# Kernel optimization log

Measured on AMD Instinct MI355X. Metric: run time of the kernel, lower is better.

## Reference

```python
import jax, jax.numpy as jnp
import numpy as np
from jax.scipy.stats import norm

N = 6144
D1, D2 = 3000, 1000
H = 128          # hardcoded hidden in VAEEncoder
LAT = 64
E = 16           # num_experts
K = 2            # top-k
NOISE_EPS = 0.01
BN_EPS = 1e-5


def setup_inputs() -> dict:
    key = jax.random.key(0)
    ks = jax.random.split(key, 24)
    xav = lambda k, i, o: jax.random.uniform(k, (i, o), jnp.float32,
                                             -np.sqrt(6.0 / (i + o)), np.sqrt(6.0 / (i + o)))
    u = jax.random.uniform(ks[0], (N, N), jnp.float32)
    adj = u / u.sum(axis=1, keepdims=True)  # row-normalized dense graph
    inp = {
        'x1': jax.random.normal(ks[1], (N, D1), jnp.float32),
        'x2': jax.random.normal(ks[2], (N, D2), jnp.float32),
        'adj': adj,
        # modality-1 VAE encoder
        'W1': xav(ks[3], D1, H), 'gamma1': jnp.ones((H,)), 'beta1': jnp.zeros((H,)),
        'Wmu1': xav(ks[4], H, LAT), 'bmu1': jnp.zeros((LAT,)),
        'Wlv1': xav(ks[5], H, LAT), 'blv1': jnp.zeros((LAT,)),
        # modality-2 VAE encoder
        'W2': xav(ks[6], D2, H), 'gamma2': jnp.ones((H,)), 'beta2': jnp.zeros((H,)),
        'Wmu2': xav(ks[7], H, LAT), 'bmu2': jnp.zeros((LAT,)),
        'Wlv2': xav(ks[8], H, LAT), 'blv2': jnp.zeros((LAT,)),
        # MoE gating (torch inits these to zero; small randn gives a non-degenerate baseline)
        'w_gate': 0.02 * jax.random.normal(ks[9], (LAT, E), jnp.float32),
        'w_noise': 0.02 * jax.random.normal(ks[10], (LAT, E), jnp.float32),
        # modality decoders
        'Wd1': xav(ks[11], LAT, LAT), 'Wfc1': xav(ks[12], LAT, D1), 'bfc1': jnp.zeros((D1,)),
        'Wd2': xav(ks[13], LAT, LAT), 'Wfc2': xav(ks[14], LAT, D2), 'bfc2': jnp.zeros((D2,)),
    }
    return inp


def _encode(x, adj, W, gamma, beta, Wmu, bmu, Wlv, blv):
    h = adj @ (x @ W)                                   # [N,H] GNN embed
    mu_b = h.mean(0)
    var_b = h.var(0)
    h = (h - mu_b) / jnp.sqrt(var_b + BN_EPS) * gamma + beta  # BatchNorm1d (train mode)
    return h @ Wmu + bmu, h @ Wlv + blv                 # mu, logvar [N,LAT]


def _cv_squared(v):
    return v.var(ddof=1) / (v.mean() ** 2 + 1e-10)


def _moe_gating(z, w_gate, w_noise, key):
    clean = z @ w_gate                                  # [N,E]
    std = jax.nn.softplus(z @ w_noise) + NOISE_EPS
    noisy = clean + jax.random.normal(key, clean.shape, clean.dtype) * std
    top_vals, top_idx = jax.lax.top_k(noisy, K + 1)     # [N,K+1]
    topk_gates = jax.nn.softmax(top_vals[:, :K], axis=1)
    rows = jnp.arange(z.shape[0])[:, None]
    gates = jnp.zeros_like(clean).at[rows, top_idx[:, :K]].set(topk_gates)
    # differentiable load estimate (prob each expert is in top-k)
    thr_in = top_vals[:, K][:, None]
    thr_out = top_vals[:, K - 1][:, None]
    is_in = noisy > thr_in
    prob = jnp.where(is_in, norm.cdf((clean - thr_in) / std), norm.cdf((clean - thr_out) / std))
    load = prob.sum(0)
    importance = gates.sum(0)
    loss = _cv_squared(importance) + _cv_squared(load)
    return gates, loss


def _decode(z, adj, Wd, Wfc, bfc):
    return (adj @ (z @ Wd)) @ Wfc + bfc                 # Decoder: mm, mm, Linear


def reference(x1, x2, adj,
              W1, gamma1, beta1, Wmu1, bmu1, Wlv1, blv1,
              W2, gamma2, beta2, Wmu2, bmu2, Wlv2, blv2,
              w_gate, w_noise,
              Wd1, Wfc1, bfc1, Wd2, Wfc2, bfc2):
    mu1, lv1 = _encode(x1, adj, W1, gamma1, beta1, Wmu1, bmu1, Wlv1, blv1)
    mu2, lv2 = _encode(x2, adj, W2, gamma2, beta2, Wmu2, bmu2, Wlv2, blv2)
    # Product of Experts over the 2 modalities
    mus = jnp.stack([mu1, mu2], 0)
    lvs = jnp.stack([lv1, lv2], 0)
    var = jnp.exp(lvs) + 1e-8
    T = 1.0 / (var + 1e-8)
    pd_mu = (mus * T).sum(0) / T.sum(0)
    pd_logvar = jnp.log(1.0 / T.sum(0) + 1e-8)
    z = pd_mu
    gates, moe_loss = _moe_gating(z, w_gate, w_noise, jax.random.key(42))
    recon1 = _decode(z, adj, Wd1, Wfc1, bfc1)
    recon2 = _decode(z, adj, Wd2, Wfc2, bfc2)
    return recon1, recon2, pd_mu, pd_logvar, gates, moe_loss
```

## Files before the change

### kernel.cpp

```cpp
#include <hip/hip_runtime.h>
#include <math.h>

#define NR    6144
#define DIM1  3000
#define DIM2  1000
#define HID   128
#define LATD  64
#define NEXP  16

typedef __bf16 bf16x8 __attribute__((ext_vector_type(8)));
typedef float  f32x4  __attribute__((ext_vector_type(4)));

__device__ __forceinline__ unsigned short f2bf_rne(float x) {
  unsigned u = __float_as_uint(x);
  u += 0x7FFFu + ((u >> 16) & 1u);
  return (unsigned short)(u >> 16);
}
__device__ __forceinline__ void split2(float v, unsigned short& h, unsigned short& l) {
  h = f2bf_rne(v);
  float hf = __uint_as_float((unsigned)h << 16);
  l = f2bf_rne(v - hf);
}

template<bool SPLIT3, bool ATOMIC>
__device__ __forceinline__ void gemm_body(
    unsigned short* __restrict__ bufA, unsigned short* __restrict__ bufB,
    const float* __restrict__ A,
    const unsigned short* __restrict__ BTh,
    const unsigned short* __restrict__ BTl,
    const float* __restrict__ bias,
    float* __restrict__ C,
    int M, int N, int K, int lda, int Kpad, int ldc,
    int bm, int bn, int k0, int kend)
{
  const int tid  = threadIdx.x;
  const int lane = tid & 63;
  const int wave = tid >> 6;
  const int wm = wave >> 1, wn = wave & 1;
  const int lrow = lane & 15, kg = lane >> 4;
  const int nsteps = (kend - k0 + 31) >> 5;

  f32x4 acc[4][4];
  #pragma unroll
  for (int f = 0; f < 4; ++f)
    #pragma unroll
    for (int g = 0; g < 4; ++g)
      #pragma unroll
      for (int j = 0; j < 4; ++j) acc[f][g][j] = 0.f;

  const int srow = tid >> 1;
  const int ks   = (tid & 1) * 16;
  const int s0   = (tid & 1) * 2;
  const float* aRow = A + (size_t)(bm + srow) * lda;
  const int gn = bn + srow;
  const bool bvalid = gn < N;
  const unsigned short* bRowH = BTh + (size_t)(bvalid ? gn : 0) * Kpad;
  const unsigned short* bRowL = SPLIT3 ? (BTl + (size_t)(bvalid ? gn : 0) * Kpad) : BTh;

  const int rx = srow & 7;
  const int wa0 = srow * 64 + (((s0 + 0) ^ rx) * 8);
  const int wa1 = srow * 64 + (((s0 + 1) ^ rx) * 8);
  const int wa2 = srow * 64 + (((s0 + 4) ^ rx) * 8);
  const int wa3 = srow * 64 + (((s0 + 5) ^ rx) * 8);

  float va[16];
  uint4 bh0 = make_uint4(0,0,0,0), bh1 = bh0, bl0 = bh0, bl1 = bh0;

  auto loadA = [&](int gk) {
    const int kb = gk + ks;
    if (kb + 16 <= kend) {
      const float4* ap = (const float4*)(aRow + kb);
      #pragma unroll
      for (int q = 0; q < 4; ++q) {
        float4 f4 = ap[q];
        va[4*q+0] = f4.x; va[4*q+1] = f4.y; va[4*q+2] = f4.z; va[4*q+3] = f4.w;
      }
    } else {
      #pragma unroll
      for (int i = 0; i < 16; ++i) va[i] = (kb + i < kend) ? aRow[kb + i] : 0.f;
    }
  };
  auto loadB = [&](int gk) {
    if (bvalid) {
      const uint4* bp = (const uint4*)(bRowH + gk + ks);
      bh0 = bp[0]; bh1 = bp[1];
      if (SPLIT3) {
        const uint4* bq = (const uint4*)(bRowL + gk + ks);
        bl0 = bq[0]; bl1 = bq[1];
      }
    }
  };

  loadA(k0);
  loadB(k0);

  for (int s = 0; s < nsteps; ++s) {
    const int gk = k0 + s * 32;

    unsigned hw[8], lw[8];
    #pragma unroll
    for (int i = 0; i < 8; ++i) {
      if (SPLIT3) {
        unsigned short h0, l0, h1, l1;
        split2(va[2*i], h0, l0);
        split2(va[2*i+1], h1, l1);
        hw[i] = (unsigned)h0 | ((unsigned)h1 << 16);
        lw[i] = (unsigned)l0 | ((unsigned)l1 << 16);
      } else {
        hw[i] = (unsigned)f2bf_rne(va[2*i]) | ((unsigned)f2bf_rne(va[2*i+1]) << 16);
        lw[i] = 0;
      }
    }

    __syncthreads();
    *(uint4*)&bufA[wa0] = make_uint4(hw[0], hw[1], hw[2], hw[3]);
    *(uint4*)&bufA[wa1] = make_uint4(hw[4], hw[5], hw[6], hw[7]);
    if (SPLIT3) {
      *(uint4*)&bufA[wa2] = make_uint4(lw[0], lw[1], lw[2], lw[3]);
      *(uint4*)&bufA[wa3] = make_uint4(lw[4], lw[5], lw[6], lw[7]);
      *(uint4*)&bufB[wa0] = bh0;
      *(uint4*)&bufB[wa1] = bh1;
      *(uint4*)&bufB[wa2] = bl0;
      *(uint4*)&bufB[wa3] = bl1;
    } else {
      *(uint4*)&bufA[wa2] = bh0;
      *(uint4*)&bufA[wa3] = bh1;
    }
    __syncthreads();

    if (s + 1 < nsteps) {
      loadA(gk + 32);
      loadB(gk + 32);
    }

    bf16x8 afh[4], bfh[4], afl[4], bfl[4];
    #pragma unroll
    for (int f = 0; f < 4; ++f) {
      const int r = wm * 64 + f * 16 + lrow;
      afh[f] = *(const bf16x8*)&bufA[r * 64 + ((kg ^ (r & 7)) * 8)];
      if (SPLIT3) afl[f] = *(const bf16x8*)&bufA[r * 64 + (((4 + kg) ^ (r & 7)) * 8)];
      const int n = wn * 64 + f * 16 + lrow;
      if (SPLIT3) {
        bfh[f] = *(const bf16x8*)&bufB[n * 64 + ((kg ^ (n & 7)) * 8)];
        bfl[f] = *(const bf16x8*)&bufB[n * 64 + (((4 + kg) ^ (n & 7)) * 8)];
      } else {
        bfh[f] = *(const bf16x8*)&bufA[n * 64 + (((4 + kg) ^ (n & 7)) * 8)];
      }
    }
    #pragma unroll
    for (int f = 0; f < 4; ++f)
      #pragma unroll
      for (int g = 0; g < 4; ++g) {
        acc[f][g] = __builtin_amdgcn_mfma_f32_16x16x32_bf16(afh[f], bfh[g], acc[f][g], 0, 0, 0);
        if constexpr (SPLIT3) {
          acc[f][g] = __builtin_amdgcn_mfma_f32_16x16x32_bf16(afl[f], bfh[g], acc[f][g], 0, 0, 0);
          acc[f][g] = __builtin_amdgcn_mfma_f32_16x16x32_bf16(afh[f], bfl[g], acc[f][g], 0, 0, 0);
        }
      }
  }

  #pragma unroll
  for (int f = 0; f < 4; ++f) {
    #pragma unroll
    for (int g = 0; g < 4; ++g) {
      const int row0 = bm + wm * 64 + f * 16 + (lane >> 4) * 4;
      const int col  = bn + wn * 64 + g * 16 + (lane & 15);
      if (col < N) {
        #pragma unroll
        for (int j = 0; j < 4; ++j) {
          const size_t idx = (size_t)(row0 + j) * ldc + col;
          if (ATOMIC) atomicAdd(&C[idx], acc[f][g][j]);
          else        C[idx] = acc[f][g][j] + (bias ? bias[col] : 0.f);
        }
      }
    }
  }
}

template<bool SPLIT3, bool ATOMIC>
__global__ __launch_bounds__(256, 3) void gemm_mfma(
    const float* __restrict__ A,
    const unsigned short* __restrict__ BTh,
    const unsigned short* __restrict__ BTl,
    const float* __restrict__ bias,
    float* __restrict__ C,
    int M, int N, int K, int lda, int Kpad, int ldc, int kchunk)
{
  __shared__ alignas(16) unsigned short bufA[128 * 64];
  __shared__ alignas(16) unsigned short bufB[SPLIT3 ? 128 * 64 : 8];
  const int k0 = blockIdx.z * kchunk;
  gemm_body<SPLIT3, ATOMIC>(bufA, bufB, A, BTh, BTl, bias, C,
                            M, N, K, lda, Kpad, ldc,
                            blockIdx.x * 128, blockIdx.y * 128,
                            k0, min(k0 + kchunk, K));
}

__global__ __launch_bounds__(256, 3) void gemm_enc(
    const float* __restrict__ x1,
    const unsigned short* __restrict__ W1h, const unsigned short* __restrict__ W1l,
    const float* __restrict__ x2,
    const unsigned short* __restrict__ W2h, const unsigned short* __restrict__ W2l,
    float* __restrict__ XW)
{
  __shared__ alignas(16) unsigned short bufA[128 * 64];
  __shared__ alignas(16) unsigned short bufB[128 * 64];
  if (blockIdx.y == 0) {
    const int k0 = blockIdx.z * 376;
    gemm_body<true, true>(bufA, bufB, x1, W1h, W1l, nullptr, XW,
                          NR, HID, DIM1, DIM1, 3008, 256,
                          blockIdx.x * 128, 0, k0, min(k0 + 376, DIM1));
  } else {
    const int k0 = blockIdx.z * 128;
    gemm_body<true, true>(bufA, bufB, x2, W2h, W2l, nullptr, XW + HID,
                          NR, HID, DIM2, DIM2, 1024, 256,
                          blockIdx.x * 128, 0, k0, min(k0 + 128, DIM2));
  }
}

__global__ __launch_bounds__(256) void transpose_split(
    const float* __restrict__ in, unsigned short* __restrict__ out_hi,
    unsigned short* __restrict__ out_lo, int K, int N, int Kpad)
{
  __shared__ float tile[32][33];
  const int k0 = blockIdx.x * 32, n0 = blockIdx.y * 32;
  const int tx = threadIdx.x & 31, ty = threadIdx.x >> 5;
  #pragma unroll
  for (int r = 0; r < 4; ++r) {
    const int k = k0 + ty + r * 8;
    tile[ty + r * 8][tx] = (k < K && n0 + tx < N) ? in[(size_t)k * N + n0 + tx] : 0.f;
  }
  __syncthreads();
  #pragma unroll
  for (int r = 0; r < 4; ++r) {
    const int nn = ty + r * 8;
    const int n = n0 + nn, k = k0 + tx;
    if (n < N && k < Kpad) {
      unsigned short h, l;
      split2(tile[tx][nn], h, l);
      out_hi[(size_t)n * Kpad + k] = h;
      if (out_lo) out_lo[(size_t)n * Kpad + k] = l;
    }
  }
}

#define BM 64
#define BN 64
#define BK 16

__global__ __launch_bounds__(256) void gemm_f32(
    const float* __restrict__ A, const float* __restrict__ B,
    const float* __restrict__ bias, float* __restrict__ C,
    int M, int N, int K, int lda, int ldb, int ldc)
{
  __shared__ float At[BK][BM + 4];
  __shared__ float Bt[BK][BN + 4];
  const int tid = threadIdx.x;
  const int tx = tid & 15;
  const int ty = tid >> 4;
  const int bm = blockIdx.x * BM;
  const int bn = blockIdx.y * BN;

  float acc[4][4] = {};

  const int ar = tid >> 2;
  const int ak = (tid & 3) * 4;
  const int bk = tid >> 4;
  const int bc = (tid & 15) * 4;

  for (int k0 = 0; k0 < K; k0 += BK) {
    {
      float4 v = make_float4(0.f, 0.f, 0.f, 0.f);
      const int gr = bm + ar;
      const int gk = k0 + ak;
      if (gr < M && gk < K) {
        const float* p = &A[(size_t)gr * lda];
        if (gk + 3 < K) v = *reinterpret_cast<const float4*>(&p[gk]);
        else {
          v.x = p[gk];
          if (gk + 1 < K) v.y = p[gk + 1];
          if (gk + 2 < K) v.z = p[gk + 2];
        }
      }
      At[ak + 0][ar] = v.x; At[ak + 1][ar] = v.y;
      At[ak + 2][ar] = v.z; At[ak + 3][ar] = v.w;
    }
    {
      float4 v = make_float4(0.f, 0.f, 0.f, 0.f);
      const int gk = k0 + bk;
      const int gc = bn + bc;
      if (gk < K) {
        const float* p = &B[(size_t)gk * ldb];
        if (gc + 3 < N) v = *reinterpret_cast<const float4*>(&p[gc]);
        else {
          if (gc     < N) v.x = p[gc];
          if (gc + 1 < N) v.y = p[gc + 1];
          if (gc + 2 < N) v.z = p[gc + 2];
        }
      }
      *reinterpret_cast<float4*>(&Bt[bk][bc]) = v;
    }
    __syncthreads();
    #pragma unroll
    for (int kk = 0; kk < BK; ++kk) {
      float4 a4 = *reinterpret_cast<const float4*>(&At[kk][ty * 4]);
      float4 b4 = *reinterpret_cast<const float4*>(&Bt[kk][tx * 4]);
      float av[4] = {a4.x, a4.y, a4.z, a4.w};
      float bv[4] = {b4.x, b4.y, b4.z, b4.w};
      #pragma unroll
      for (int i = 0; i < 4; ++i)
        #pragma unroll
        for (int j = 0; j < 4; ++j)
          acc[i][j] = fmaf(av[i], bv[j], acc[i][j]);
    }
    __syncthreads();
  }

  #pragma unroll
  for (int i = 0; i < 4; ++i) {
    const int row = bm + ty * 4 + i;
    if (row >= M) continue;
    #pragma unroll
    for (int j = 0; j < 4; ++j) {
      const int col = bn + tx * 4 + j;
      if (col < N) {
        float v = acc[i][j];
        if (bias) v += bias[col];
        C[(size_t)row * ldc + col] = v;
      }
    }
  }
}

__global__ __launch_bounds__(256) void bnstats_kernel(
    const float* __restrict__ H2, float* __restrict__ ssum, float* __restrict__ ssq)
{
  const int c = threadIdx.x;
  const int r0 = blockIdx.x * 12;
  float s = 0.f, q = 0.f;
  #pragma unroll
  for (int i = 0; i < 12; ++i) {
    float v = H2[(size_t)(r0 + i) * 256 + c];
    s += v;
    q = fmaf(v, v, q);
  }
  atomicAdd(&ssum[c], s);
  atomicAdd(&ssq[c], q);
}

__global__ __launch_bounds__(256) void mulv_kernel(
    const float* __restrict__ H2, const float* __restrict__ ssum, const float* __restrict__ ssq,
    const float* __restrict__ g1, const float* __restrict__ b1,
    const float* __restrict__ Wmu1, const float* __restrict__ bmu1,
    const float* __restrict__ Wlv1, const float* __restrict__ blv1,
    const float* __restrict__ g2, const float* __restrict__ b2,
    const float* __restrict__ Wmu2, const float* __restrict__ bmu2,
    const float* __restrict__ Wlv2, const float* __restrict__ blv2,
    float* __restrict__ pd_mu_out, float* __restrict__ pd_lv_out, float* __restrict__ z_out)
{
  __shared__ float hn[4][256];
  const int tid = threadIdx.x;
  const int r0 = blockIdx.x * 4;

  for (int idx = tid; idx < 1024; idx += 256) {
    const int rr = idx >> 8;
    const int c  = idx & 255;
    const float mean = ssum[c] * (1.0f / 6144.0f);
    const float var  = ssq[c] * (1.0f / 6144.0f) - mean * mean;
    const float rstd = 1.0f / sqrtf(var + 1e-5f);
    const float gamma = (c < HID) ? g1[c] : g2[c - HID];
    const float beta  = (c < HID) ? b1[c] : b2[c - HID];
    const float v = H2[(size_t)(r0 + rr) * 256 + c];
    hn[rr][c] = (v - mean) * rstd * gamma + beta;
  }
  __syncthreads();

  const int rr = tid >> 6;
  const int j  = tid & 63;
  float mu1 = bmu1[j], lv1 = blv1[j], mu2 = bmu2[j], lv2 = blv2[j];
  #pragma unroll 4
  for (int k = 0; k < HID; ++k) {
    const float h1 = hn[rr][k];
    const float h2 = hn[rr][HID + k];
    mu1 = fmaf(h1, Wmu1[k * LATD + j], mu1);
    lv1 = fmaf(h1, Wlv1[k * LATD + j], lv1);
    mu2 = fmaf(h2, Wmu2[k * LATD + j], mu2);
    lv2 = fmaf(h2, Wlv2[k * LATD + j], lv2);
  }
  const float var1 = expf(lv1) + 1e-8f;
  const float var2 = expf(lv2) + 1e-8f;
  const float T1 = 1.0f / (var1 + 1e-8f);
  const float T2 = 1.0f / (var2 + 1e-8f);
  const float denom = T1 + T2;
  const float pmu = (mu1 * T1 + mu2 * T2) / denom;
  const float plv = logf(1.0f / denom + 1e-8f);
  const size_t o = (size_t)(r0 + rr) * LATD + j;
  pd_mu_out[o] = pmu;
  pd_lv_out[o] = plv;
  z_out[o]     = pmu;
}

__device__ __forceinline__ unsigned rotl32(unsigned x, int r) {
  return (x << r) | (x >> (32 - r));
}

__device__ float threefry_normal(unsigned i) {
  const unsigned ks0 = 0u;
  const unsigned ks1 = 42u;
  const unsigned ks2 = 0x1BD11BDAu ^ 0u ^ 42u;
  unsigned x0 = 0u + ks0;
  unsigned x1 = i + ks1;

  #define TF_ROUND(r) { x0 += x1; x1 = rotl32(x1, r); x1 ^= x0; }
  TF_ROUND(13) TF_ROUND(15) TF_ROUND(26) TF_ROUND(6)
  x0 += ks1; x1 += ks2 + 1u;
  TF_ROUND(17) TF_ROUND(29) TF_ROUND(16) TF_ROUND(24)
  x0 += ks2; x1 += ks0 + 2u;
  TF_ROUND(13) TF_ROUND(15) TF_ROUND(26) TF_ROUND(6)
  x0 += ks0; x1 += ks1 + 3u;
  TF_ROUND(17) TF_ROUND(29) TF_ROUND(16) TF_ROUND(24)
  x0 += ks1; x1 += ks2 + 4u;
  TF_ROUND(13) TF_ROUND(15) TF_ROUND(26) TF_ROUND(6)
  x0 += ks2; x1 += ks0 + 5u;
  #undef TF_ROUND

  const unsigned bits = x0 ^ x1;

  const unsigned fb = (bits >> 9) | 0x3F800000u;
  const float u01 = __uint_as_float(fb) - 1.0f;
  const float minval = -0.99999994f;
  float u = fmaf(u01, 2.0f, minval);
  u = fmaxf(minval, u);

  float w = -log1pf(-u * u);
  float p;
  if (w < 5.0f) {
    w = w - 2.5f;
    p = 2.81022636e-08f;
    p = fmaf(p, w, 3.43273939e-07f);
    p = fmaf(p, w, -3.5233877e-06f);
    p = fmaf(p, w, -4.39150654e-06f);
    p = fmaf(p, w, 0.00021858087f);
    p = fmaf(p, w, -0.00125372503f);
    p = fmaf(p, w, -0.00417768164f);
    p = fmaf(p, w, 0.246640727f);
    p = fmaf(p, w, 1.50140941f);
  } else {
    w = sqrtf(w) - 3.0f;
    p = -0.000200214257f;
    p = fmaf(p, w, 0.000100950558f);
    p = fmaf(p, w, 0.00134934322f);
    p = fmaf(p, w, -0.00367342844f);
    p = fmaf(p, w, 0.00573950773f);
    p = fmaf(p, w, -0.0076224613f);
    p = fmaf(p, w, 0.00943887047f);
    p = fmaf(p, w, 1.00167406f);
    p = fmaf(p, w, 2.83297682f);
  }
  return 1.4142135f * (p * u);
}

__global__ __launch_bounds__(64) void gating_kernel(
    const float* __restrict__ z, const float* __restrict__ w_gate,
    const float* __restrict__ w_noise, float* __restrict__ gates_out,
    float* __restrict__ importance, float* __restrict__ loadv)
{
  __shared__ float zt[64][65];
  __shared__ float wg[64][16];
  __shared__ float wn[64][16];
  __shared__ float imp_s[16];
  __shared__ float load_s[16];

  const int tid = threadIdx.x;
  const int r0 = blockIdx.x * 64;

  for (int idx = tid; idx < 1024; idx += 64) {
    wg[idx >> 4][idx & 15] = w_gate[idx];
    wn[idx >> 4][idx & 15] = w_noise[idx];
  }
  for (int idx = tid; idx < 4096; idx += 64) {
    const int rr = idx >> 6, c = idx & 63;
    zt[rr][c] = z[(size_t)(r0 + rr) * 64 + c];
  }
  if (tid < 16) { imp_s[tid] = 0.f; load_s[tid] = 0.f; }
  __syncthreads();

  const int r = r0 + tid;
  float clean[16], noisy[16], stdv[16];
  #pragma unroll
  for (int e = 0; e < NEXP; ++e) {
    float c = 0.f, n = 0.f;
    #pragma unroll 8
    for (int k = 0; k < 64; ++k) {
      const float zv = zt[tid][k];
      c = fmaf(zv, wg[k][e], c);
      n = fmaf(zv, wn[k][e], n);
    }
    clean[e] = c;
    const float sp = fmaxf(n, 0.f) + log1pf(expf(-fabsf(n)));
    stdv[e] = sp + 0.01f;
    const float eps = threefry_normal((unsigned)r * 16u + (unsigned)e);
    noisy[e] = fmaf(eps, stdv[e], c);
  }

  float v0 = -1e30f, v1 = -1e30f, v2 = -1e30f;
  int i0 = 0, i1 = 0;
  #pragma unroll
  for (int e = 0; e < NEXP; ++e) {
    const float v = noisy[e];
    if (v > v0)      { v2 = v1; v1 = v0; i1 = i0; v0 = v; i0 = e; }
    else if (v > v1) { v2 = v1; v1 = v; i1 = e; }
    else if (v > v2) { v2 = v; }
  }

  const float e1 = expf(v1 - v0);
  const float inv = 1.0f / (1.0f + e1);
  const float g0 = inv;
  const float g1v = e1 * inv;

  float lacc[16];
  #pragma unroll
  for (int e = 0; e < NEXP; ++e) {
    const float gv = (e == i0) ? g0 : ((e == i1) ? g1v : 0.f);
    gates_out[(size_t)r * NEXP + e] = gv;
    const float thr = (noisy[e] > v2) ? v2 : v1;
    const float x = (clean[e] - thr) / stdv[e];
    lacc[e] = 0.5f * erfcf(-0.70710678f * x);
  }
  atomicAdd(&imp_s[i0], g0);
  atomicAdd(&imp_s[i1], g1v);
  #pragma unroll
  for (int e = 0; e < NEXP; ++e) atomicAdd(&load_s[e], lacc[e]);
  __syncthreads();
  if (tid < 16) {
    atomicAdd(&importance[tid], imp_s[tid]);
    atomicAdd(&loadv[tid], load_s[tid]);
  }
}

__global__ void loss_kernel(const float* __restrict__ imp, const float* __restrict__ ld,
                            float* __restrict__ out)
{
  if (threadIdx.x == 0 && blockIdx.x == 0) {
    float mi = 0.f, ml = 0.f;
    for (int e = 0; e < NEXP; ++e) { mi += imp[e]; ml += ld[e]; }
    mi *= (1.0f / 16.0f);
    ml *= (1.0f / 16.0f);
    float vi = 0.f, vl = 0.f;
    for (int e = 0; e < NEXP; ++e) {
      const float di = imp[e] - mi;
      const float dl = ld[e] - ml;
      vi = fmaf(di, di, vi);
      vl = fmaf(dl, dl, vl);
    }
    vi *= (1.0f / 15.0f);
    vl *= (1.0f / 15.0f);
    out[0] = vi / (mi * mi + 1e-10f) + vl / (ml * ml + 1e-10f);
  }
}

extern "C" void kernel_launch(void* const* d_in, const int* in_sizes, int n_in,
                              void* d_out, int out_size, void* d_ws, size_t ws_size,
                              hipStream_t stream)
{
  const float* x1     = (const float*)d_in[0];
  const float* x2     = (const float*)d_in[1];
  const float* adj    = (const float*)d_in[2];
  const float* W1     = (const float*)d_in[3];
  const float* gamma1 = (const float*)d_in[4];
  const float* beta1  = (const float*)d_in[5];
  const float* Wmu1   = (const float*)d_in[6];
  const float* bmu1   = (const float*)d_in[7];
  const float* Wlv1   = (const float*)d_in[8];
  const float* blv1   = (const float*)d_in[9];
  const float* W2     = (const float*)d_in[10];
  const float* gamma2 = (const float*)d_in[11];
  const float* beta2  = (const float*)d_in[12];
  const float* Wmu2   = (const float*)d_in[13];
  const float* bmu2   = (const float*)d_in[14];
  const float* Wlv2   = (const float*)d_in[15];
  const float* blv2   = (const float*)d_in[16];
  const float* w_gate = (const float*)d_in[17];
  const float* w_noise= (const float*)d_in[18];
  const float* Wd1    = (const float*)d_in[19];
  const float* Wfc1   = (const float*)d_in[20];
  const float* bfc1   = (const float*)d_in[21];
  const float* Wd2    = (const float*)d_in[22];
  const float* Wfc2   = (const float*)d_in[23];
  const float* bfc2   = (const float*)d_in[24];

  float* out = (float*)d_out;
  float* recon1 = out;
  float* recon2 = out + (size_t)NR * DIM1;
  float* pd_mu  = recon2 + (size_t)NR * DIM2;
  float* pd_lv  = pd_mu + (size_t)NR * LATD;
  float* gates  = pd_lv + (size_t)NR * LATD;
  float* loss   = gates + (size_t)NR * NEXP;

  char* wsb = (char*)d_ws;
  const size_t o_XW   = 0;
  const size_t o_H2   = o_XW   + 6291456;
  const size_t o_z    = o_H2   + 6291456;
  const size_t o_ZD   = o_z    + 1572864;
  const size_t o_AZ   = o_ZD   + 3145728;
  const size_t o_XWTh = o_AZ   + 3145728;
  const size_t o_XWTl = o_XWTh + 3145728;
  const size_t o_W1Th = o_XWTl + 3145728;
  const size_t o_W1Tl = o_W1Th + 770048;
  const size_t o_W2Th = o_W1Tl + 770048;
  const size_t o_W2Tl = o_W2Th + 262144;
  const size_t o_ZDTh = o_W2Tl + 262144;
  const size_t o_F1Th = o_ZDTh + 1572864;
  const size_t o_F2Th = o_F1Th + 384000;
  const size_t o_stat = o_F2Th + 128000;
  const size_t need   = o_stat + 2176;

  const dim3 blk(256);

  if (ws_size >= need) {
    float* XW   = (float*)(wsb + o_XW);
    float* H2   = (float*)(wsb + o_H2);
    float* zbuf = (float*)(wsb + o_z);
    float* ZD   = (float*)(wsb + o_ZD);
    float* AZ   = (float*)(wsb + o_AZ);
    unsigned short* XWTh = (unsigned short*)(wsb + o_XWTh);
    unsigned short* XWTl = (unsigned short*)(wsb + o_XWTl);
    unsigned short* W1Th = (unsigned short*)(wsb + o_W1Th);
    unsigned short* W1Tl = (unsigned short*)(wsb + o_W1Tl);
    unsigned short* W2Th = (unsigned short*)(wsb + o_W2Th);
    unsigned short* W2Tl = (unsigned short*)(wsb + o_W2Tl);
    unsigned short* ZDTh = (unsigned short*)(wsb + o_ZDTh);
    unsigned short* F1Th = (unsigned short*)(wsb + o_F1Th);
    unsigned short* F2Th = (unsigned short*)(wsb + o_F2Th);
    float* ssum = (float*)(wsb + o_stat);
    float* ssq  = ssum + 256;
    float* imp  = ssq + 256;
    float* ldv  = imp + 16;

    hipMemsetAsync(XW, 0, 6291456 * 2, stream);
    hipMemsetAsync(AZ, 0, 3145728, stream);
    hipMemsetAsync(ssum, 0, 2176, stream);

    transpose_split<<<dim3(94, 4), blk, 0, stream>>>(W1, W1Th, W1Tl, DIM1, HID, 3008);
    transpose_split<<<dim3(32, 4), blk, 0, stream>>>(W2, W2Th, W2Tl, DIM2, HID, 1024);
    transpose_split<<<dim3(2, 94), blk, 0, stream>>>(Wfc1, F1Th, nullptr, LATD, DIM1, 64);
    transpose_split<<<dim3(2, 32), blk, 0, stream>>>(Wfc2, F2Th, nullptr, LATD, DIM2, 64);

    gemm_enc<<<dim3(48, 2, 8), blk, 0, stream>>>(x1, W1Th, W1Tl, x2, W2Th, W2Tl, XW);

    transpose_split<<<dim3(192, 8), blk, 0, stream>>>(XW, XWTh, XWTl, NR, 256, NR);

    gemm_mfma<true, true><<<dim3(48, 2, 8), blk, 0, stream>>>(
        adj, XWTh, XWTl, nullptr, H2, NR, 256, NR, NR, NR, 256, 768);

    bnstats_kernel<<<512, blk, 0, stream>>>(H2, ssum, ssq);
    mulv_kernel<<<NR / 4, blk, 0, stream>>>(H2, ssum, ssq,
        gamma1, beta1, Wmu1, bmu1, Wlv1, blv1,
        gamma2, beta2, Wmu2, bmu2, Wlv2, blv2,
        pd_mu, pd_lv, zbuf);

    gating_kernel<<<NR / 64, 64, 0, stream>>>(zbuf, w_gate, w_noise, gates, imp, ldv);
    loss_kernel<<<1, 64, 0, stream>>>(imp, ldv, loss);

    gemm_f32<<<dim3(96, 1), blk, 0, stream>>>(zbuf, Wd1, nullptr, ZD,        NR, LATD, LATD, LATD, LATD, 128);
    gemm_f32<<<dim3(96, 1), blk, 0, stream>>>(zbuf, Wd2, nullptr, ZD + LATD, NR, LATD, LATD, LATD, LATD, 128);
    transpose_split<<<dim3(192, 4), blk, 0, stream>>>(ZD, ZDTh, nullptr, NR, 128, NR);
    gemm_mfma<false, true><<<dim3(48, 1, 16), blk, 0, stream>>>(
        adj, ZDTh, nullptr, nullptr, AZ, NR, 128, NR, NR, NR, 128, 384);
    gemm_mfma<false, false><<<dim3(48, 24, 1), blk, 0, stream>>>(
        AZ, F1Th, nullptr, bfc1, recon1, NR, DIM1, LATD, 128, 64, DIM1, 64);
    gemm_mfma<false, false><<<dim3(48, 8, 1), blk, 0, stream>>>(
        AZ + LATD, F2Th, nullptr, bfc2, recon2, NR, DIM2, LATD, 128, 64, DIM2, 64);
    return;
  }

  float* ws   = (float*)d_ws;
  float* XW   = ws;
  float* H2   = ws + 1572864;
  float* zbuf = ws + 3145728;
  float* ZD   = ws + 3538944;
  float* AZ   = ws + 4325376;
  float* ssum = ws + 5111808;
  float* ssq  = ws + 5112064;
  float* imp  = ws + 5112320;
  float* ldv  = ws + 5112336;

  hipMemsetAsync(ssum, 0, 544 * sizeof(float), stream);

  gemm_f32<<<dim3(NR / BM, 2), blk, 0, stream>>>(x1, W1, nullptr, XW,        NR, HID, DIM1, DIM1, HID, 256);
  gemm_f32<<<dim3(NR / BM, 2), blk, 0, stream>>>(x2, W2, nullptr, XW + HID,  NR, HID, DIM2, DIM2, HID, 256);
  gemm_f32<<<dim3(NR / BM, 4), blk, 0, stream>>>(adj, XW, nullptr, H2, NR, 256, NR, NR, 256, 256);
  bnstats_kernel<<<512, blk, 0, stream>>>(H2, ssum, ssq);
  mulv_kernel<<<NR / 4, blk, 0, stream>>>(H2, ssum, ssq,
                                          gamma1, beta1, Wmu1, bmu1, Wlv1, blv1,
                                          gamma2, beta2, Wmu2, bmu2, Wlv2, blv2,
                                          pd_mu, pd_lv, zbuf);
  gating_kernel<<<NR / 64, 64, 0, stream>>>(zbuf, w_gate, w_noise, gates, imp, ldv);
  loss_kernel<<<1, 64, 0, stream>>>(imp, ldv, loss);
  gemm_f32<<<dim3(NR / BM, 1), blk, 0, stream>>>(zbuf, Wd1, nullptr, ZD,        NR, LATD, LATD, LATD, LATD, 128);
  gemm_f32<<<dim3(NR / BM, 1), blk, 0, stream>>>(zbuf, Wd2, nullptr, ZD + LATD, NR, LATD, LATD, LATD, LATD, 128);
  gemm_f32<<<dim3(NR / BM, 2), blk, 0, stream>>>(adj, ZD, nullptr, AZ, NR, 128, NR, NR, 128, 128);
  gemm_f32<<<dim3(NR / BM, (DIM1 + BN - 1) / BN), blk, 0, stream>>>(AZ,        Wfc1, bfc1, recon1, NR, DIM1, LATD, 128, DIM1, DIM1);
  gemm_f32<<<dim3(NR / BM, (DIM2 + BN - 1) / BN), blk, 0, stream>>>(AZ + LATD, Wfc2, bfc2, recon2, NR, DIM2, LATD, 128, DIM2, DIM2);
}
```

Baseline: 418.3 us.

## Double-buffer LDS tiles in MFMA GEMM to drop one barrier per k-step

Makes the shared-memory A/B tiles double-buffered, alternating by step parity, so each k-step needs only one barrier instead of two. The next global loads are issued before the LDS stores, and a raw s_barrier with an explicit lgkmcnt wait replaces __syncthreads. This doubles LDS use per block, so the occupancy hint in launch_bounds drops from 3 to 2 blocks per CU, which may reduce latency hiding.

```diff
diff --git a/kernel.cpp b/kernel.cpp
--- a/kernel.cpp
+++ b/kernel.cpp
@@ -33,6 +33,7 @@
     int M, int N, int K, int lda, int Kpad, int ldc,
     int bm, int bn, int k0, int kend)
 {
+  constexpr int BUFSZ = 128 * 64;
   const int tid  = threadIdx.x;
   const int lane = tid & 63;
   const int wave = tid >> 6;
@@ -95,7 +96,8 @@
   loadB(k0);
 
   for (int s = 0; s < nsteps; ++s) {
-    const int gk = k0 + s * 32;
+    unsigned short* bA = bufA + (s & 1) * BUFSZ;
+    unsigned short* bB = SPLIT3 ? (bufB + (s & 1) * BUFSZ) : bA;
 
     unsigned hw[8], lw[8];
     #pragma unroll
@@ -111,40 +113,44 @@
         lw[i] = 0;
       }
     }
-
-    __syncthreads();
-    *(uint4*)&bufA[wa0] = make_uint4(hw[0], hw[1], hw[2], hw[3]);
-    *(uint4*)&bufA[wa1] = make_uint4(hw[4], hw[5], hw[6], hw[7]);
+    uint4 wb0 = bh0, wb1 = bh1, wb2 = bl0, wb3 = bl1;
+
+    if (s + 1 < nsteps) {
+      loadA(k0 + (s + 1) * 32);
+      loadB(k0 + (s + 1) * 32);
+    }
+
+    *(uint4*)&bA[wa0] = make_uint4(hw[0], hw[1], hw[2], hw[3]);
+    *(uint4*)&bA[wa1] = make_uint4(hw[4], hw[5], hw[6], hw[7]);
     if (SPLIT3) {
-      *(uint4*)&bufA[wa2] = make_uint4(lw[0], lw[1], lw[2], lw[3]);
-      *(uint4*)&bufA[wa3] = make_uint4(lw[4], lw[5], lw[6], lw[7]);
-      *(uint4*)&bufB[wa0] = bh0;
-      *(uint4*)&bufB[wa1] = bh1;
-      *(uint4*)&bufB[wa2] = bl0;
-      *(uint4*)&bufB[wa3] = bl1;
+      *(uint4*)&bA[wa2] = make_uint4(lw[0], lw[1], lw[2], lw[3]);
+      *(uint4*)&bA[wa3] = make_uint4(lw[4], lw[5], lw[6], lw[7]);
+      *(uint4*)&bB[wa0] = wb0;
+      *(uint4*)&bB[wa1] = wb1;
+      *(uint4*)&bB[wa2] = wb2;
+      *(uint4*)&bB[wa3] = wb3;
     } else {
-      *(uint4*)&bufA[wa2] = bh0;
-      *(uint4*)&bufA[wa3] = bh1;
-    }
-    __syncthreads();
-
-    if (s + 1 < nsteps) {
-      loadA(gk + 32);
-      loadB(gk + 32);
-    }
+      *(uint4*)&bA[wa2] = wb0;
+      *(uint4*)&bA[wa3] = wb1;
+    }
+
+    asm volatile("s_waitcnt lgkmcnt(0)" ::: "memory");
+    __builtin_amdgcn_sched_barrier(0);
+    __builtin_amdgcn_s_barrier();
+    asm volatile("" ::: "memory");
 
     bf16x8 afh[4], bfh[4], afl[4], bfl[4];
     #pragma unroll
     for (int f = 0; f < 4; ++f) {
       const int r = wm * 64 + f * 16 + lrow;
-      afh[f] = *(const bf16x8*)&bufA[r * 64 + ((kg ^ (r & 7)) * 8)];
-      if (SPLIT3) afl[f] = *(const bf16x8*)&bufA[r * 64 + (((4 + kg) ^ (r & 7)) * 8)];
+      afh[f] = *(const bf16x8*)&bA[r * 64 + ((kg ^ (r & 7)) * 8)];
+      if (SPLIT3) afl[f] = *(const bf16x8*)&bA[r * 64 + (((4 + kg) ^ (r & 7)) * 8)];
       const int n = wn * 64 + f * 16 + lrow;
       if (SPLIT3) {
-        bfh[f] = *(const bf16x8*)&bufB[n * 64 + ((kg ^ (n & 7)) * 8)];
-        bfl[f] = *(const bf16x8*)&bufB[n * 64 + (((4 + kg) ^ (n & 7)) * 8)];
+        bfh[f] = *(const bf16x8*)&bB[n * 64 + ((kg ^ (n & 7)) * 8)];
+        bfl[f] = *(const bf16x8*)&bB[n * 64 + (((4 + kg) ^ (n & 7)) * 8)];
       } else {
-        bfh[f] = *(const bf16x8*)&bufA[n * 64 + (((4 + kg) ^ (n & 7)) * 8)];
+        bfh[f] = *(const bf16x8*)&bA[n * 64 + (((4 + kg) ^ (n & 7)) * 8)];
       }
     }
     #pragma unroll
@@ -178,7 +184,7 @@
 }
 
 template<bool SPLIT3, bool ATOMIC>
-__global__ __launch_bounds__(256, 3) void gemm_mfma(
+__global__ __launch_bounds__(256, 2) void gemm_mfma(
     const float* __restrict__ A,
     const unsigned short* __restrict__ BTh,
     const unsigned short* __restrict__ BTl,
@@ -186,8 +192,8 @@
     float* __restrict__ C,
     int M, int N, int K, int lda, int Kpad, int ldc, int kchunk)
 {
-  __shared__ alignas(16) unsigned short bufA[128 * 64];
-  __shared__ alignas(16) unsigned short bufB[SPLIT3 ? 128 * 64 : 8];
+  __shared__ alignas(16) unsigned short bufA[2 * 128 * 64];
+  __shared__ alignas(16) unsigned short bufB[SPLIT3 ? 2 * 128 * 64 : 8];
   const int k0 = blockIdx.z * kchunk;
   gemm_body<SPLIT3, ATOMIC>(bufA, bufB, A, BTh, BTl, bias, C,
                             M, N, K, lda, Kpad, ldc,
@@ -195,15 +201,15 @@
                             k0, min(k0 + kchunk, K));
 }
 
-__global__ __launch_bounds__(256, 3) void gemm_enc(
+__global__ __launch_bounds__(256, 2) void gemm_enc(
     const float* __restrict__ x1,
     const unsigned short* __restrict__ W1h, const unsigned short* __restrict__ W1l,
     const float* __restrict__ x2,
     const unsigned short* __restrict__ W2h, const unsigned short* __restrict__ W2l,
     float* __restrict__ XW)
 {
-  __shared__ alignas(16) unsigned short bufA[128 * 64];
-  __shared__ alignas(16) unsigned short bufB[128 * 64];
+  __shared__ alignas(16) unsigned short bufA[2 * 128 * 64];
+  __shared__ alignas(16) unsigned short bufB[2 * 128 * 64];
   if (blockIdx.y == 0) {
     const int k0 = blockIdx.z * 376;
     gemm_body<true, true>(bufA, bufB, x1, W1h, W1l, nullptr, XW,
```

Measured after the change: 466.3 us. +11.5%, slower.

## Double-buffer A prefetch two steps ahead and use packed bf16 convert

Applied to the files above, without the earlier changes.

The GEMM mainloop now keeps two register buffers for the fp32 A tile and prefetches A two K-steps ahead (B one step ahead), so global load latency gets more time to hide behind the MFMA work. The manual RNE float-to-bf16 splitting is replaced with the hardware v_cvt_pk_bf16_f32 instruction, which cuts VALU work in the hi/lo split path. __syncthreads is replaced with raw s_barrier calls wrapped in sched_barrier fences plus an explicit lgkmcnt wait. The cost is roughly 16 more VGPRs per thread, which could lower occupancy, and the inline asm depends on the ISA providing that convert instruction.

```diff
diff --git a/kernel.cpp b/kernel.cpp
--- a/kernel.cpp
+++ b/kernel.cpp
@@ -20,6 +20,11 @@
   h = f2bf_rne(v);
   float hf = __uint_as_float((unsigned)h << 16);
   l = f2bf_rne(v - hf);
+}
+__device__ __forceinline__ unsigned cvt_pk_bf16(float a, float b) {
+  unsigned r;
+  asm("v_cvt_pk_bf16_f32 %0, %1, %2" : "=v"(r) : "v"(a), "v"(b));
+  return r;
 }
 
 template<bool SPLIT3, bool ATOMIC>
@@ -63,10 +68,10 @@
   const int wa2 = srow * 64 + (((s0 + 4) ^ rx) * 8);
   const int wa3 = srow * 64 + (((s0 + 5) ^ rx) * 8);
 
-  float va[16];
+  float vaA[16], vaB[16];
   uint4 bh0 = make_uint4(0,0,0,0), bh1 = bh0, bl0 = bh0, bl1 = bh0;
 
-  auto loadA = [&](int gk) {
+  auto loadAinto = [&](float* va, int gk) {
     const int kb = gk + ks;
     if (kb + 16 <= kend) {
       const float4* ap = (const float4*)(aRow + kb);
@@ -91,28 +96,24 @@
     }
   };
 
-  loadA(k0);
-  loadB(k0);
-
-  for (int s = 0; s < nsteps; ++s) {
-    const int gk = k0 + s * 32;
-
+  auto substep = [&](float* va, int s) {
     unsigned hw[8], lw[8];
     #pragma unroll
     for (int i = 0; i < 8; ++i) {
+      hw[i] = cvt_pk_bf16(va[2*i], va[2*i+1]);
       if (SPLIT3) {
-        unsigned short h0, l0, h1, l1;
-        split2(va[2*i], h0, l0);
-        split2(va[2*i+1], h1, l1);
-        hw[i] = (unsigned)h0 | ((unsigned)h1 << 16);
-        lw[i] = (unsigned)l0 | ((unsigned)l1 << 16);
+        const float h0 = __uint_as_float(hw[i] << 16);
+        const float h1 = __uint_as_float(hw[i] & 0xFFFF0000u);
+        lw[i] = cvt_pk_bf16(va[2*i] - h0, va[2*i+1] - h1);
       } else {
-        hw[i] = (unsigned)f2bf_rne(va[2*i]) | ((unsigned)f2bf_rne(va[2*i+1]) << 16);
         lw[i] = 0;
       }
     }
 
-    __syncthreads();
+    __builtin_amdgcn_sched_barrier(0);
+    __builtin_amdgcn_s_barrier();
+    __builtin_amdgcn_sched_barrier(0);
+
     *(uint4*)&bufA[wa0] = make_uint4(hw[0], hw[1], hw[2], hw[3]);
     *(uint4*)&bufA[wa1] = make_uint4(hw[4], hw[5], hw[6], hw[7]);
     if (SPLIT3) {
@@ -126,12 +127,14 @@
       *(uint4*)&bufA[wa2] = bh0;
       *(uint4*)&bufA[wa3] = bh1;
     }
-    __syncthreads();
-
-    if (s + 1 < nsteps) {
-      loadA(gk + 32);
-      loadB(gk + 32);
-    }
+
+    asm volatile("s_waitcnt lgkmcnt(0)" ::: "memory");
+    __builtin_amdgcn_sched_barrier(0);
+    __builtin_amdgcn_s_barrier();
+    __builtin_amdgcn_sched_barrier(0);
+
+    if (s + 1 < nsteps) loadB(k0 + (s + 1) * 32);
+    if (s + 2 < nsteps) loadAinto(va, k0 + (s + 2) * 32);
 
     bf16x8 afh[4], bfh[4], afl[4], bfl[4];
     #pragma unroll
@@ -157,6 +160,15 @@
           acc[f][g] = __builtin_amdgcn_mfma_f32_16x16x32_bf16(afh[f], bfl[g], acc[f][g], 0, 0, 0);
         }
       }
+  };
+
+  loadAinto(vaA, k0);
+  loadB(k0);
+  if (nsteps > 1) loadAinto(vaB, k0 + 32);
+
+  for (int s = 0; s < nsteps; ++s) {
+    if ((s & 1) == 0) substep(vaA, s);
+    else              substep(vaB, s);
   }
 
   #pragma unroll
```

Result: slower. 1.072 ms (+156.3%).
